# Optimization experiments

Hardware: AMD Instinct MI355X
Metric: run time of the kernel (lower is better)

## Reference

```python
import jax, jax.numpy as jnp
import numpy as np

B, S, DM, DC = 16, 4096, 1280, 768
N_AOE, N_IMG, N_DELTA = 16, 16, 16
ANAT_GATE, DIS_GATE, DELTA_SCALE = 0.5, 0.5, 1.0


def setup_inputs() -> dict:
    key = jax.random.key(0)
    ks = jax.random.split(key, 9)
    def lin(k, fan_in, fan_out):
        return jax.random.normal(k, (fan_in, fan_out), jnp.float32) / np.sqrt(fan_in)
    return {
        "hidden_states": jax.random.normal(ks[0], (B, S, DM), jnp.float32),
        "encoder_hidden_states": jax.random.normal(ks[1], (B, N_AOE + N_IMG + N_DELTA, DC), jnp.float32),
        "w_q": lin(ks[2], DM, DM),
        "w_k": lin(ks[3], DC, DM),
        "w_v": lin(ks[4], DC, DM),
        "w_k_dis": lin(ks[5], DC, DM),
        "w_v_dis": lin(ks[6], DC, DM),
        "w_out": lin(ks[7], DM, DM),
        "b_out": jnp.zeros((DM,), jnp.float32),
        "n_heads": 8,
    }


def _heads(x, h):
    b, s, d = x.shape
    return x.reshape(b, s, h, d // h).transpose(0, 2, 1, 3)  # [B,H,S,dh]


def _attend(q, k, v, scale):
    # q:[B,H,Sq,dh], k/v:[B,H,Sk,dh], Sk small (16)
    scores = jnp.einsum("bhqd,bhkd->bhqk", q, k) * scale
    probs = jax.nn.softmax(scores, axis=-1)
    return jnp.einsum("bhqk,bhkd->bhqd", probs, v)


def reference(hidden_states, encoder_hidden_states, w_q, w_k, w_v,
              w_k_dis, w_v_dis, w_out, b_out, n_heads):
    residual = hidden_states
    dh = DM // n_heads
    scale = 1.0 / np.sqrt(dh)

    dis_tok = encoder_hidden_states[:, :N_AOE, :]
    anat_tok = encoder_hidden_states[:, N_AOE:N_AOE + N_IMG, :]
    delta_tok = encoder_hidden_states[:, -N_DELTA:, :]

    q = _heads(hidden_states @ w_q, n_heads)
    z_anat = _attend(q, _heads(anat_tok @ w_k, n_heads), _heads(anat_tok @ w_v, n_heads), scale)
    z_dis = _attend(q, _heads(dis_tok @ w_k_dis, n_heads), _heads(dis_tok @ w_v_dis, n_heads), scale)
    z_delta = _attend(q, _heads(delta_tok @ w_k_dis, n_heads), _heads(delta_tok @ w_v_dis, n_heads), scale)

    z = ANAT_GATE * z_anat + DIS_GATE * z_dis + DELTA_SCALE * z_delta
    out = z.transpose(0, 2, 1, 3).reshape(hidden_states.shape[0], -1, DM)
    out = out @ w_out + b_out  # to_out[0]; to_out[1] dropout = identity in eval
    return out + residual  # residual_connection, rescale_output_factor=1.0
```

## Files before the change

### kernel.cpp

```cpp
#include <hip/hip_runtime.h>
#include <hip/hip_bf16.h>

#define B_ 16
#define S_ 4096
#define DM_ 1280
#define DC_ 768
#define NC_ 384
#define SCALE_ 0.07905694150420949f

typedef __attribute__((ext_vector_type(8))) short bf16x8;
typedef __attribute__((ext_vector_type(4))) float f32x4;
typedef __attribute__((ext_vector_type(4))) unsigned short u16x4;

#define S_BARRIER() asm volatile("s_barrier" ::: "memory")
#define WAIT_VM(n) asm volatile("s_waitcnt vmcnt(" #n ")" ::: "memory")
#define WAIT_LGKM0() asm volatile("s_waitcnt lgkmcnt(0)" ::: "memory")

__device__ __forceinline__ unsigned short f2bf(float f) {
    unsigned int u = __builtin_bit_cast(unsigned int, f);
    u = (u + 0x7FFFu + ((u >> 16) & 1u)) >> 16;
    return (unsigned short)u;
}

__device__ __forceinline__ bf16x8 pack8(float4 x0, float4 x1) {
    bf16x8 a;
    a[0] = __builtin_bit_cast(short, __float2bfloat16(x0.x));
    a[1] = __builtin_bit_cast(short, __float2bfloat16(x0.y));
    a[2] = __builtin_bit_cast(short, __float2bfloat16(x0.z));
    a[3] = __builtin_bit_cast(short, __float2bfloat16(x0.w));
    a[4] = __builtin_bit_cast(short, __float2bfloat16(x1.x));
    a[5] = __builtin_bit_cast(short, __float2bfloat16(x1.y));
    a[6] = __builtin_bit_cast(short, __float2bfloat16(x1.z));
    a[7] = __builtin_bit_cast(short, __float2bfloat16(x1.w));
    return a;
}

__device__ __forceinline__ void gload16(const void* g, void* l) {
    __builtin_amdgcn_global_load_lds(
        (const __attribute__((address_space(1))) void*)g,
        (__attribute__((address_space(3))) void*)l, 16, 0, 0);
}

__device__ __forceinline__ void tcvt_body(const float* __restrict__ in,
                                          unsigned short* __restrict__ out,
                                          int R, int C, int bx, int by, int tid) {
    __shared__ float tile[32][33];
    int c0 = bx * 32, r0 = by * 32;
    int tx = tid & 31, ty = tid >> 5;
    for (int i = ty; i < 32; i += 8)
        tile[i][tx] = in[(size_t)(r0 + i) * C + c0 + tx];
    __syncthreads();
    for (int i = ty; i < 32; i += 8)
        out[(size_t)(c0 + i) * R + r0 + tx] = f2bf(tile[tx][i]);
}

__global__ __launch_bounds__(256)
void k_prep(const float* __restrict__ wq, const float* __restrict__ wk,
            const float* __restrict__ wv, const float* __restrict__ wkd,
            const float* __restrict__ wvd, const float* __restrict__ wout,
            unsigned short* __restrict__ wq_bf, unsigned short* __restrict__ wTk,
            unsigned short* __restrict__ wTv, unsigned short* __restrict__ wTkd,
            unsigned short* __restrict__ wTvd, unsigned short* __restrict__ woutT) {
    int bid = blockIdx.x, tid = threadIdx.x;
    if (bid < 1600) {
        int i = bid * 256 + tid;
        float4 v = ((const float4*)wq)[i];
        u16x4 o = { f2bf(v.x), f2bf(v.y), f2bf(v.z), f2bf(v.w) };
        ((u16x4*)wq_bf)[i] = o;
    } else if (bid < 2560) {
        int r = bid - 1600; tcvt_body(wk,  wTk,  DC_, DM_, r % 40, r / 40, tid);
    } else if (bid < 3520) {
        int r = bid - 2560; tcvt_body(wv,  wTv,  DC_, DM_, r % 40, r / 40, tid);
    } else if (bid < 4480) {
        int r = bid - 3520; tcvt_body(wkd, wTkd, DC_, DM_, r % 40, r / 40, tid);
    } else if (bid < 5440) {
        int r = bid - 4480; tcvt_body(wvd, wTvd, DC_, DM_, r % 40, r / 40, tid);
    } else {
        int r = bid - 5440; tcvt_body(wout, woutT, DM_, DM_, r % 40, r / 40, tid);
    }
}

__global__ __launch_bounds__(256)
void k_au2(const float* __restrict__ enc,
           const unsigned short* __restrict__ wTk, const unsigned short* __restrict__ wTv,
           const unsigned short* __restrict__ wTkd, const unsigned short* __restrict__ wTvd,
           const unsigned short* __restrict__ wqbf, const unsigned short* __restrict__ woutT,
           unsigned short* __restrict__ At2, unsigned short* __restrict__ Ut2) {
    __shared__ unsigned short kvLds[16 * 168];
    int bid0 = blockIdx.x;
    bool isA = bid0 < 384;
    int bid = isA ? bid0 : bid0 - 384;
    int b = bid & 15, r_ = bid >> 4, x = r_ >> 3, h = r_ & 7;
    int tid = threadIdx.x, w = tid >> 6, l = tid & 63, l15 = l & 15, l4 = l >> 4;
    int xh = x * 8 + h;
    int tok0 = (x == 0) ? 16 : ((x == 1) ? 0 : 32);
    const unsigned short* wTproj = isA ? ((x == 0) ? wTk : wTkd)
                                       : ((x == 0) ? wTv : wTvd);
    const unsigned short* wmat = isA ? wqbf : woutT;
    float postscale = isA ? SCALE_ : ((x == 2) ? 1.0f : 0.5f);
    f32x4 zero = {0.f, 0.f, 0.f, 0.f};

    {
        const float* ap = enc + ((size_t)(b * 48 + tok0 + l15)) * DC_;
        f32x4 pacc[3];
        #pragma unroll
        for (int i = 0; i < 3; i++) pacc[i] = zero;
        for (int kk = 0; kk < 24; kk++) {
            const float4* hp = (const float4*)(ap + kk * 32 + l4 * 8);
            bf16x8 af = pack8(hp[0], hp[1]);
            int i = 0;
            for (int t2 = w; t2 < 10; t2 += 4, i++) {
                int n0 = h * 160 + t2 * 16;
                bf16x8 bf = *(const bf16x8*)(wTproj + (size_t)(n0 + l15) * DC_ + kk * 32 + l4 * 8);
                pacc[i] = __builtin_amdgcn_mfma_f32_16x16x32_bf16(af, bf, pacc[i], 0, 0, 0);
            }
        }
        int i = 0;
        for (int t2 = w; t2 < 10; t2 += 4, i++) {
            #pragma unroll
            for (int r = 0; r < 4; r++)
                kvLds[(l4 * 4 + r) * 168 + t2 * 16 + l15] = f2bf(pacc[i][r]);
        }
    }
    __syncthreads();

    bf16x8 bfr[5];
    #pragma unroll
    for (int kk = 0; kk < 5; kk++)
        bfr[kk] = *(const bf16x8*)&kvLds[l15 * 168 + kk * 32 + l4 * 8];

    for (int tt = 0; tt < 20; tt++) {
        int d0 = w * 320 + tt * 16;
        f32x4 acc = zero;
        if (isA) {
            #pragma unroll
            for (int kk = 0; kk < 5; kk++) {
                bf16x8 af = *(const bf16x8*)(wmat + (size_t)(d0 + l15) * DM_ + h * 160 + kk * 32 + l4 * 8);
                acc = __builtin_amdgcn_mfma_f32_16x16x32_bf16(af, bfr[kk], acc, 0, 0, 0);
            }
            int c = xh * 16 + l15;
            u16x4 pk;
            #pragma unroll
            for (int r = 0; r < 4; r++) pk[r] = f2bf(acc[r] * postscale);
            *(u16x4*)(At2 + ((size_t)(b * 40 + (d0 >> 5)) * NC_ + c) * 32 + (d0 & 31) + l4 * 4) = pk;
        } else {
            #pragma unroll
            for (int kk = 0; kk < 5; kk++) {
                bf16x8 af = *(const bf16x8*)(wmat + (size_t)(d0 + l15) * DM_ + h * 160 + kk * 32 + l4 * 8);
                acc = __builtin_amdgcn_mfma_f32_16x16x32_bf16(bfr[kk], af, acc, 0, 0, 0);
            }
            int e = d0 + l15;
            u16x4 pk;
            #pragma unroll
            for (int r = 0; r < 4; r++) pk[r] = f2bf(acc[r] * postscale);
            *(u16x4*)(Ut2 + ((size_t)(b * 12 + (xh >> 1)) * DM_ + e) * 32 + (xh & 1) * 16 + l4 * 4) = pk;
        }
    }
}

__global__ __launch_bounds__(256, 2)
void k_fused(const float* __restrict__ hid, const unsigned short* __restrict__ At2,
             const unsigned short* __restrict__ Ut2, const float* __restrict__ bo,
             float* __restrict__ out) {
    __shared__ char smem[81920];
    unsigned short* Apnl = (unsigned short*)smem;
    char* Hlds = smem + 49152;
    unsigned short* Ulds2 = (unsigned short*)(smem + 49152);
    int bid = blockIdx.x;
    int orig = (bid & 7) * 128 + (bid >> 3);
    int b = orig >> 6, st = orig & 63;
    int s0 = st * 64;
    int tid = threadIdx.x, w = tid >> 6, l = tid & 63, l15 = l & 15, l4 = l >> 4;
    int rdsw = (l4 ^ ((l15 >> 1) & 3)) * 8;
    const unsigned short* Ab = At2 + (size_t)b * 40 * NC_ * 32;
    const float* hsrc = hid + ((size_t)b * S_ + s0) * DM_;
    f32x4 zero = {0.f, 0.f, 0.f, 0.f};

    {
        f32x4 acc[4][6];
        #pragma unroll
        for (int si = 0; si < 4; si++)
            #pragma unroll
            for (int cj = 0; cj < 6; cj++) acc[si][cj] = zero;

        auto stageA = [&](int kk, int ab) {
            const unsigned short* slab = Ab + (size_t)kk * (NC_ * 32);
            #pragma unroll
            for (int i = 0; i < 6; i++) {
                int idx = i * 256 + tid;
                int c = idx >> 2, m = (idx & 3) ^ ((c >> 1) & 3);
                gload16(slab + (size_t)c * 32 + m * 8, smem + ab * 24576 + idx * 16);
            }
        };
        auto stageH = [&](int kk, int hb) {
            #pragma unroll
            for (int i = 0; i < 2; i++) {
                int idx = i * 256 + tid;
                int r = idx >> 3, sg = (idx & 7) ^ (r & 7);
                gload16(hsrc + (size_t)r * DM_ + kk * 32 + sg * 4, Hlds + hb * 8192 + idx * 16);
            }
        };
        auto compute = [&](int ab, int hb) {
            bf16x8 hpk[4];
            #pragma unroll
            for (int si = 0; si < 4; si++) {
                int r = si * 16 + l15;
                float4 lo = *(const float4*)(Hlds + hb * 8192 + r * 128 + (((2 * l4) ^ (l15 & 7)) * 16));
                float4 hi = *(const float4*)(Hlds + hb * 8192 + r * 128 + (((2 * l4 + 1) ^ (l15 & 7)) * 16));
                hpk[si] = pack8(lo, hi);
            }
            __builtin_amdgcn_s_setprio(1);
            #pragma unroll
            for (int cj = 0; cj < 6; cj++) {
                bf16x8 af = *(const bf16x8*)&Apnl[ab * 12288 + (w * 96 + cj * 16 + l15) * 32 + rdsw];
                #pragma unroll
                for (int si = 0; si < 4; si++)
                    acc[si][cj] = __builtin_amdgcn_mfma_f32_16x16x32_bf16(af, hpk[si], acc[si][cj], 0, 0, 0);
            }
            __builtin_amdgcn_s_setprio(0);
        };
        auto SITER = [&](int kk) {
            stageA(kk + 1, (kk + 1) & 1);
            stageH(kk + 2, (kk + 2) % 3);
            WAIT_VM(10);
            S_BARRIER();
            compute(kk & 1, kk % 3);
            WAIT_LGKM0();
            S_BARRIER();
        };

        stageA(0, 0); stageH(0, 0); stageH(1, 1);
        for (int k0 = 0; k0 < 36; k0 += 6) {
            SITER(k0 + 0); SITER(k0 + 1); SITER(k0 + 2);
            SITER(k0 + 3); SITER(k0 + 4); SITER(k0 + 5);
        }
        SITER(36); SITER(37);
        stageA(39, 1);
        WAIT_VM(8);
        S_BARRIER();
        compute(0, 38 % 3);
        WAIT_LGKM0();
        S_BARRIER();
        WAIT_VM(0);
        S_BARRIER();
        compute(1, 39 % 3);
        WAIT_LGKM0();
        S_BARRIER();

        #pragma unroll
        for (int si = 0; si < 4; si++) {
            int s_l = si * 16 + l15;
            #pragma unroll
            for (int cj = 0; cj < 6; cj++) {
                float v0 = acc[si][cj][0], v1 = acc[si][cj][1], v2 = acc[si][cj][2], v3 = acc[si][cj][3];
                float mx = fmaxf(fmaxf(v0, v1), fmaxf(v2, v3));
                mx = fmaxf(mx, __shfl_xor(mx, 16));
                mx = fmaxf(mx, __shfl_xor(mx, 32));
                float e0 = __expf(v0 - mx), e1 = __expf(v1 - mx), e2 = __expf(v2 - mx), e3 = __expf(v3 - mx);
                float sm = e0 + e1 + e2 + e3;
                sm += __shfl_xor(sm, 16);
                sm += __shfl_xor(sm, 32);
                float rs = 1.0f / sm;
                u16x4 pk = { f2bf(e0 * rs), f2bf(e1 * rs), f2bf(e2 * rs), f2bf(e3 * rs) };
                int c = w * 96 + cj * 16 + l4 * 4;
                int chunk = ((c & 31) >> 3) ^ ((s_l >> 1) & 3);
                *(u16x4*)(smem + (c >> 5) * 4096 + s_l * 64 + chunk * 16 + (l4 & 1) * 8) = pk;
            }
        }
    }
    __syncthreads();

    const unsigned short* Ub = Ut2 + (size_t)b * 12 * DM_ * 32;
    auto stageU = [&](int kk2, int ec, int buf) {
        const unsigned short* slab = Ub + ((size_t)kk2 * DM_ + ec * 256) * 32;
        #pragma unroll
        for (int i = 0; i < 4; i++) {
            int idx = i * 256 + tid;
            int r = idx >> 2, m = (idx & 3) ^ ((r >> 1) & 3);
            gload16(slab + (size_t)r * 32 + m * 8, (char*)Ulds2 + buf * 16384 + idx * 16);
        }
    };

    for (int ec = 0; ec < 5; ec++) {
        f32x4 accp[4][4];
        #pragma unroll
        for (int si = 0; si < 4; si++)
            #pragma unroll
            for (int ej = 0; ej < 4; ej++) accp[si][ej] = zero;

        stageU(0, ec, 0);
        for (int kk2 = 0; kk2 < 12; kk2++) {
            if (kk2 < 11) {
                stageU(kk2 + 1, ec, (kk2 + 1) & 1);
                WAIT_VM(4);
            } else {
                WAIT_VM(0);
            }
            S_BARRIER();
            int buf = kk2 & 1;
            bf16x8 uf[4], pf[4];
            #pragma unroll
            for (int ej = 0; ej < 4; ej++)
                uf[ej] = *(const bf16x8*)&Ulds2[buf * 8192 + (w * 64 + ej * 16 + l15) * 32 + rdsw];
            #pragma unroll
            for (int si = 0; si < 4; si++) {
                int s_l = si * 16 + l15;
                pf[si] = *(const bf16x8*)(smem + kk2 * 4096 + s_l * 64 + ((l4 ^ ((s_l >> 1) & 3)) * 16));
            }
            __builtin_amdgcn_s_setprio(1);
            #pragma unroll
            for (int si = 0; si < 4; si++)
                #pragma unroll
                for (int ej = 0; ej < 4; ej++)
                    accp[si][ej] = __builtin_amdgcn_mfma_f32_16x16x32_bf16(uf[ej], pf[si], accp[si][ej], 0, 0, 0);
            __builtin_amdgcn_s_setprio(0);
            WAIT_LGKM0();
            S_BARRIER();
        }

        #pragma unroll
        for (int ej = 0; ej < 4; ej++) {
            int e0c = ec * 256 + w * 64 + ej * 16 + l4 * 4;
            float4 b4 = *(const float4*)(bo + e0c);
            #pragma unroll
            for (int si = 0; si < 4; si++) {
                int srow = s0 + si * 16 + l15;
                size_t off = ((size_t)b * S_ + srow) * DM_ + e0c;
                float4 h4 = *(const float4*)(hid + off);
                f32x4 a = accp[si][ej];
                float4 o4;
                o4.x = a[0] + b4.x + h4.x;
                o4.y = a[1] + b4.y + h4.y;
                o4.z = a[2] + b4.z + h4.z;
                o4.w = a[3] + b4.w + h4.w;
                *(float4*)(out + off) = o4;
            }
        }
    }
}

extern "C" void kernel_launch(void* const* d_in, const int* in_sizes, int n_in,
                              void* d_out, int out_size, void* d_ws, size_t ws_size,
                              hipStream_t stream) {
    const float* hid  = (const float*)d_in[0];
    const float* enc  = (const float*)d_in[1];
    const float* wq   = (const float*)d_in[2];
    const float* wk   = (const float*)d_in[3];
    const float* wv   = (const float*)d_in[4];
    const float* wkd  = (const float*)d_in[5];
    const float* wvd  = (const float*)d_in[6];
    const float* wout = (const float*)d_in[7];
    const float* bo   = (const float*)d_in[8];
    float* out = (float*)d_out;

    char* ws = (char*)d_ws;
    unsigned short* At2    = (unsigned short*)(ws);
    unsigned short* Ut2    = (unsigned short*)(ws + 15728640);
    unsigned short* wq_bf  = (unsigned short*)(ws + 31457280);
    unsigned short* woutT  = (unsigned short*)(ws + 34734080);
    unsigned short* wTk    = (unsigned short*)(ws + 38010880);
    unsigned short* wTv    = (unsigned short*)(ws + 39976960);
    unsigned short* wTkd   = (unsigned short*)(ws + 41943040);
    unsigned short* wTvd   = (unsigned short*)(ws + 43909120);

    k_prep<<<7040, 256, 0, stream>>>(wq, wk, wv, wkd, wvd, wout,
                                     wq_bf, wTk, wTv, wTkd, wTvd, woutT);
    k_au2<<<768, 256, 0, stream>>>(enc, wTk, wTv, wTkd, wTvd, wq_bf, woutT, At2, Ut2);
    k_fused<<<1024, 256, 0, stream>>>(hid, At2, Ut2, bo, out);
}
```

Before: 400.1 us.

## Repartition fused kernel so each wave owns 16 rows and keeps probabilities in registers

Changes the work split in the fused kernel. Each wave now computes all 384 score columns for its own 16 query rows, instead of a 96-column slice across all 64 rows. The softmax probabilities are moved into MFMA B-fragment layout with cross-lane shuffles and kept in registers, so the LDS round trip for P goes away. The second GEMM now loads 64-column U slabs into LDS with no double buffering and has each wave reuse them against its register-resident P. The cost is many more LDS A-fragment reads per wave in the first GEMM, more register pressure, and a load-then-wait pattern with no overlap in the output GEMM.

```diff
diff --git a/kernel.cpp b/kernel.cpp
--- a/kernel.cpp
+++ b/kernel.cpp
@@ -159,13 +159,12 @@
 }
 
 __global__ __launch_bounds__(256, 2)
-void k_fused(const float* __restrict__ hid, const unsigned short* __restrict__ At2,
-             const unsigned short* __restrict__ Ut2, const float* __restrict__ bo,
-             float* __restrict__ out) {
-    __shared__ char smem[81920];
+void k_fused2(const float* __restrict__ hid, const unsigned short* __restrict__ At2,
+              const unsigned short* __restrict__ Ut2, const float* __restrict__ bo,
+              float* __restrict__ out) {
+    __shared__ char smem[73728];
     unsigned short* Apnl = (unsigned short*)smem;
     char* Hlds = smem + 49152;
-    unsigned short* Ulds2 = (unsigned short*)(smem + 49152);
     int bid = blockIdx.x;
     int orig = (bid & 7) * 128 + (bid >> 3);
     int b = orig >> 6, st = orig & 63;
@@ -176,12 +175,12 @@
     const float* hsrc = hid + ((size_t)b * S_ + s0) * DM_;
     f32x4 zero = {0.f, 0.f, 0.f, 0.f};
 
+    uint4 pf4[12];
+
     {
-        f32x4 acc[4][6];
-        #pragma unroll
-        for (int si = 0; si < 4; si++)
-            #pragma unroll
-            for (int cj = 0; cj < 6; cj++) acc[si][cj] = zero;
+        f32x4 acc[24];
+        #pragma unroll
+        for (int g = 0; g < 24; g++) acc[g] = zero;
 
         auto stageA = [&](int kk, int ab) {
             const unsigned short* slab = Ab + (size_t)kk * (NC_ * 32);
@@ -201,21 +200,15 @@
             }
         };
         auto compute = [&](int ab, int hb) {
-            bf16x8 hpk[4];
-            #pragma unroll
-            for (int si = 0; si < 4; si++) {
-                int r = si * 16 + l15;
-                float4 lo = *(const float4*)(Hlds + hb * 8192 + r * 128 + (((2 * l4) ^ (l15 & 7)) * 16));
-                float4 hi = *(const float4*)(Hlds + hb * 8192 + r * 128 + (((2 * l4 + 1) ^ (l15 & 7)) * 16));
-                hpk[si] = pack8(lo, hi);
-            }
+            int r = w * 16 + l15;
+            float4 lo = *(const float4*)(Hlds + hb * 8192 + r * 128 + (((2 * l4) ^ (l15 & 7)) * 16));
+            float4 hi = *(const float4*)(Hlds + hb * 8192 + r * 128 + (((2 * l4 + 1) ^ (l15 & 7)) * 16));
+            bf16x8 hpk = pack8(lo, hi);
             __builtin_amdgcn_s_setprio(1);
             #pragma unroll
-            for (int cj = 0; cj < 6; cj++) {
-                bf16x8 af = *(const bf16x8*)&Apnl[ab * 12288 + (w * 96 + cj * 16 + l15) * 32 + rdsw];
-                #pragma unroll
-                for (int si = 0; si < 4; si++)
-                    acc[si][cj] = __builtin_amdgcn_mfma_f32_16x16x32_bf16(af, hpk[si], acc[si][cj], 0, 0, 0);
+            for (int g = 0; g < 24; g++) {
+                bf16x8 af = *(const bf16x8*)&Apnl[ab * 12288 + (g * 16 + l15) * 32 + rdsw];
+                acc[g] = __builtin_amdgcn_mfma_f32_16x16x32_bf16(af, hpk, acc[g], 0, 0, 0);
             }
             __builtin_amdgcn_s_setprio(0);
         };
@@ -247,94 +240,89 @@
         WAIT_LGKM0();
         S_BARRIER();
 
-        #pragma unroll
-        for (int si = 0; si < 4; si++) {
-            int s_l = si * 16 + l15;
-            #pragma unroll
-            for (int cj = 0; cj < 6; cj++) {
-                float v0 = acc[si][cj][0], v1 = acc[si][cj][1], v2 = acc[si][cj][2], v3 = acc[si][cj][3];
-                float mx = fmaxf(fmaxf(v0, v1), fmaxf(v2, v3));
-                mx = fmaxf(mx, __shfl_xor(mx, 16));
-                mx = fmaxf(mx, __shfl_xor(mx, 32));
-                float e0 = __expf(v0 - mx), e1 = __expf(v1 - mx), e2 = __expf(v2 - mx), e3 = __expf(v3 - mx);
-                float sm = e0 + e1 + e2 + e3;
-                sm += __shfl_xor(sm, 16);
-                sm += __shfl_xor(sm, 32);
-                float rs = 1.0f / sm;
-                u16x4 pk = { f2bf(e0 * rs), f2bf(e1 * rs), f2bf(e2 * rs), f2bf(e3 * rs) };
-                int c = w * 96 + cj * 16 + l4 * 4;
-                int chunk = ((c & 31) >> 3) ^ ((s_l >> 1) & 3);
-                *(u16x4*)(smem + (c >> 5) * 4096 + s_l * 64 + chunk * 16 + (l4 & 1) * 8) = pk;
-            }
+        unsigned int Wp[24][2];
+        #pragma unroll
+        for (int g = 0; g < 24; g++) {
+            float v0 = acc[g][0], v1 = acc[g][1], v2 = acc[g][2], v3 = acc[g][3];
+            float mx = fmaxf(fmaxf(v0, v1), fmaxf(v2, v3));
+            mx = fmaxf(mx, __shfl_xor(mx, 16));
+            mx = fmaxf(mx, __shfl_xor(mx, 32));
+            float e0 = __expf(v0 - mx), e1 = __expf(v1 - mx), e2 = __expf(v2 - mx), e3 = __expf(v3 - mx);
+            float sm = e0 + e1 + e2 + e3;
+            sm += __shfl_xor(sm, 16);
+            sm += __shfl_xor(sm, 32);
+            float rs = 1.0f / sm;
+            Wp[g][0] = (unsigned int)f2bf(e0 * rs) | ((unsigned int)f2bf(e1 * rs) << 16);
+            Wp[g][1] = (unsigned int)f2bf(e2 * rs) | ((unsigned int)f2bf(e3 * rs) << 16);
+        }
+        int srcA = (((2 * l4) & 3) << 4) | l15;
+        int srcB = (((2 * l4 + 1) & 3) << 4) | l15;
+        bool hiG = (l4 >= 2);
+        #pragma unroll
+        for (int K = 0; K < 12; K++) {
+            int g0 = 2 * K, g1 = 2 * K + 1;
+            unsigned int a0 = (unsigned int)__shfl((int)Wp[g0][0], srcA);
+            unsigned int a1 = (unsigned int)__shfl((int)Wp[g0][1], srcA);
+            unsigned int b0 = (unsigned int)__shfl((int)Wp[g0][0], srcB);
+            unsigned int b1 = (unsigned int)__shfl((int)Wp[g0][1], srcB);
+            unsigned int c0 = (unsigned int)__shfl((int)Wp[g1][0], srcA);
+            unsigned int c1 = (unsigned int)__shfl((int)Wp[g1][1], srcA);
+            unsigned int d0 = (unsigned int)__shfl((int)Wp[g1][0], srcB);
+            unsigned int d1 = (unsigned int)__shfl((int)Wp[g1][1], srcB);
+            uint4 fr;
+            fr.x = hiG ? c0 : a0;
+            fr.y = hiG ? c1 : a1;
+            fr.z = hiG ? d0 : b0;
+            fr.w = hiG ? d1 : b1;
+            pf4[K] = fr;
         }
     }
     __syncthreads();
 
     const unsigned short* Ub = Ut2 + (size_t)b * 12 * DM_ * 32;
-    auto stageU = [&](int kk2, int ec, int buf) {
-        const unsigned short* slab = Ub + ((size_t)kk2 * DM_ + ec * 256) * 32;
-        #pragma unroll
-        for (int i = 0; i < 4; i++) {
-            int idx = i * 256 + tid;
-            int r = idx >> 2, m = (idx & 3) ^ ((r >> 1) & 3);
-            gload16(slab + (size_t)r * 32 + m * 8, (char*)Ulds2 + buf * 16384 + idx * 16);
-        }
-    };
-
-    for (int ec = 0; ec < 5; ec++) {
-        f32x4 accp[4][4];
-        #pragma unroll
-        for (int si = 0; si < 4; si++)
-            #pragma unroll
-            for (int ej = 0; ej < 4; ej++) accp[si][ej] = zero;
-
-        stageU(0, ec, 0);
+    unsigned short* Usm = (unsigned short*)smem;
+    int srow = s0 + w * 16 + l15;
+
+    for (int ecb = 0; ecb < 20; ecb++) {
+        #pragma unroll
         for (int kk2 = 0; kk2 < 12; kk2++) {
-            if (kk2 < 11) {
-                stageU(kk2 + 1, ec, (kk2 + 1) & 1);
-                WAIT_VM(4);
-            } else {
-                WAIT_VM(0);
-            }
-            S_BARRIER();
-            int buf = kk2 & 1;
-            bf16x8 uf[4], pf[4];
-            #pragma unroll
-            for (int ej = 0; ej < 4; ej++)
-                uf[ej] = *(const bf16x8*)&Ulds2[buf * 8192 + (w * 64 + ej * 16 + l15) * 32 + rdsw];
-            #pragma unroll
-            for (int si = 0; si < 4; si++) {
-                int s_l = si * 16 + l15;
-                pf[si] = *(const bf16x8*)(smem + kk2 * 4096 + s_l * 64 + ((l4 ^ ((s_l >> 1) & 3)) * 16));
-            }
-            __builtin_amdgcn_s_setprio(1);
-            #pragma unroll
-            for (int si = 0; si < 4; si++)
-                #pragma unroll
-                for (int ej = 0; ej < 4; ej++)
-                    accp[si][ej] = __builtin_amdgcn_mfma_f32_16x16x32_bf16(uf[ej], pf[si], accp[si][ej], 0, 0, 0);
-            __builtin_amdgcn_s_setprio(0);
-            WAIT_LGKM0();
-            S_BARRIER();
-        }
+            const unsigned short* slab = Ub + ((size_t)kk2 * DM_ + ecb * 64) * 32;
+            int r = tid >> 2, m = (tid & 3) ^ ((r >> 1) & 3);
+            gload16(slab + (size_t)r * 32 + m * 8, smem + kk2 * 4096 + tid * 16);
+        }
+        WAIT_VM(0);
+        S_BARRIER();
+
+        f32x4 acc2[4];
+        #pragma unroll
+        for (int ej = 0; ej < 4; ej++) acc2[ej] = zero;
+        __builtin_amdgcn_s_setprio(1);
+        #pragma unroll
+        for (int kk2 = 0; kk2 < 12; kk2++) {
+            bf16x8 pfr = __builtin_bit_cast(bf16x8, pf4[kk2]);
+            #pragma unroll
+            for (int ej = 0; ej < 4; ej++) {
+                bf16x8 uf = *(const bf16x8*)&Usm[kk2 * 2048 + (ej * 16 + l15) * 32 + rdsw];
+                acc2[ej] = __builtin_amdgcn_mfma_f32_16x16x32_bf16(uf, pfr, acc2[ej], 0, 0, 0);
+            }
+        }
+        __builtin_amdgcn_s_setprio(0);
+        WAIT_LGKM0();
+        S_BARRIER();
 
         #pragma unroll
         for (int ej = 0; ej < 4; ej++) {
-            int e0c = ec * 256 + w * 64 + ej * 16 + l4 * 4;
+            int e0c = ecb * 64 + ej * 16 + l4 * 4;
             float4 b4 = *(const float4*)(bo + e0c);
-            #pragma unroll
-            for (int si = 0; si < 4; si++) {
-                int srow = s0 + si * 16 + l15;
-                size_t off = ((size_t)b * S_ + srow) * DM_ + e0c;
-                float4 h4 = *(const float4*)(hid + off);
-                f32x4 a = accp[si][ej];
-                float4 o4;
-                o4.x = a[0] + b4.x + h4.x;
-                o4.y = a[1] + b4.y + h4.y;
-                o4.z = a[2] + b4.z + h4.z;
-                o4.w = a[3] + b4.w + h4.w;
-                *(float4*)(out + off) = o4;
-            }
+            size_t off = ((size_t)b * S_ + srow) * DM_ + e0c;
+            float4 h4 = *(const float4*)(hid + off);
+            f32x4 a = acc2[ej];
+            float4 o4;
+            o4.x = a[0] + b4.x + h4.x;
+            o4.y = a[1] + b4.y + h4.y;
+            o4.z = a[2] + b4.z + h4.z;
+            o4.w = a[3] + b4.w + h4.w;
+            *(float4*)(out + off) = o4;
         }
     }
 }
@@ -366,5 +354,5 @@
     k_prep<<<7040, 256, 0, stream>>>(wq, wk, wv, wkd, wvd, wout,
                                      wq_bf, wTk, wTv, wTkd, wTvd, woutT);
     k_au2<<<768, 256, 0, stream>>>(enc, wTk, wTv, wTkd, wTvd, wq_bf, woutT, At2, Ut2);
-    k_fused<<<1024, 256, 0, stream>>>(hid, At2, Ut2, bo, out);
-}
+    k_fused2<<<1024, 256, 0, stream>>>(hid, At2, Ut2, bo, out);
+}
```

Result: no change. 395.0 us (-1.3%).
